# Performance work log

Hardware: AMD Instinct MI355X
Metric: run time of the kernel (lower is better)

Reference implementation:

```python
import jax, jax.numpy as jnp
import numpy as np

K = 5       # local window size (odd)
G = 4       # groups

def _gconv1x1(x, w):
    # grouped 1x1 conv: x (b,c,h,w), w (g, c_out_g, c_in_g) -> (b,g,c_out_g,h,w)
    b, c, h, wd = x.shape
    g, co, ci = w.shape
    xg = x.reshape(b, g, ci, h, wd)
    return jnp.einsum('bgihw,goi->bgohw', xg, w)

def _windows(f, h, w):
    # f: (b,g,n,h+2p,w+2p) -> (b,g,n,h,w,K*K), row-major over (ki,kj)
    # matches torch .unfold(2,K,1).unfold(3,K,1).view(..., -1)
    return jnp.stack([f[..., i:i + h, j:j + w]
                      for i in range(K) for j in range(K)], axis=-1)

def setup_inputs() -> dict:
    key = jax.random.key(0)
    k1, k2, k3, k4 = jax.random.split(key, 4)
    x = jax.random.normal(k1, (2, 128, 96, 96), dtype=jnp.float32)
    wq = jax.random.normal(k2, (G, 32, 32), dtype=jnp.float32) * 0.1
    wk = jax.random.normal(k3, (G, 32, 32), dtype=jnp.float32) * 0.1
    wv = jax.random.normal(k4, (G, 32, 32), dtype=jnp.float32) * 0.1
    return {"x": x, "wq": wq, "wk": wk, "wv": wv}

def reference(x, wq, wk, wv):
    b, c, h, w = x.shape
    p = K // 2
    # query: plain grouped 1x1 conv, broadcast over window dim
    q = _gconv1x1(x, wq)[..., None]                      # (b,g,n,h,w,1)
    # key/value: reflect-pad (1x1 conv commutes with padding, same as torch's
    # Conv2d(..., padding=k//2, padding_mode='reflect'))
    xp = jnp.pad(x, ((0, 0), (0, 0), (p, p), (p, p)), mode='reflect')
    kf = _gconv1x1(xp, wk)                               # (b,g,n,h+2p,w+2p)
    vf = _gconv1x1(xp, wv)
    kwin = _windows(kf, h, w)                            # (b,g,n,h,w,K*K)
    vwin = _windows(vf, h, w)
    attn = jax.nn.softmax(q * kwin, axis=-1)             # per-channel window softmax
    y = (attn * vwin).sum(-1)                            # (b,g,n,h,w)
    return y.reshape(b, -1, h, w)                        # (b, c_out, h, w)
```

## Files before the change

kernel.cpp:

```cpp
#include <hip/hip_runtime.h>


#define HW 96
#define RG 12
#define CSTR 36
#define PXN 9216

typedef _Float16 half8  __attribute__((ext_vector_type(8)));
typedef _Float16 half2v __attribute__((ext_vector_type(2)));
typedef float    float4v __attribute__((ext_vector_type(4)));
typedef unsigned int uint4v __attribute__((ext_vector_type(4)));

__device__ __forceinline__ int refl(int i) {
    i = (i < 0) ? -i : i;
    i = (i > 95) ? (190 - i) : i;
    return i;
}

__global__ __launch_bounds__(256) void conv_qkv(
    const float* __restrict__ x, const float* __restrict__ wq,
    const float* __restrict__ wk, const float* __restrict__ wv,
    _Float16* __restrict__ qp, _Float16* __restrict__ kp, _Float16* __restrict__ vp)
{
    const int tid  = threadIdx.x;
    const int g = blockIdx.y, b = blockIdx.z;
    const int lane = tid & 63, wid = tid >> 6;
    const int col  = lane & 15;
    const int quad = lane >> 4;
    const int koff = quad * 8;
    const int pxw  = blockIdx.x * 128 + wid * 32;
    const float* xg = x + (size_t)(b * 128 + g * 32) * PXN;
    const size_t plane = (size_t)(b * 4 + g) * PXN * 32;

    const float* wsrc[3] = {wq, wk, wv};
    half8 frag[6];
    #pragma unroll
    for (int T = 0; T < 6; T++) {
        const float* wr = wsrc[T >> 1] + (g * 32 + (T & 1) * 16 + col) * 32 + koff;
        float sc = (T < 2) ? 1.44269504f : 1.0f;
        #pragma unroll
        for (int j = 0; j < 8; j++) frag[T][j] = (_Float16)(wr[j] * sc);
    }

    _Float16* outp[3] = {qp, kp, vp};
    #pragma unroll
    for (int s = 0; s < 2; s++) {
        int apx = pxw + s * 16 + col;
        half8 a;
        #pragma unroll
        for (int j = 0; j < 8; j++)
            a[j] = (_Float16)xg[(koff + j) * PXN + apx];
        #pragma unroll
        for (int T = 0; T < 6; T++) {
            float4v d = {0.f, 0.f, 0.f, 0.f};
            d = __builtin_amdgcn_mfma_f32_16x16x32_f16(a, frag[T], d, 0, 0, 0);
            _Float16* pl = outp[T >> 1];
            #pragma unroll
            for (int r = 0; r < 4; r++) {
                int dpx = pxw + s * 16 + quad * 4 + r;
                pl[plane + (size_t)dpx * 32 + (T & 1) * 16 + col] = (_Float16)d[r];
            }
        }
    }
}

__global__ __launch_bounds__(256) void attn(
    const _Float16* __restrict__ qp, const _Float16* __restrict__ kp,
    const _Float16* __restrict__ vp, float* __restrict__ out)
{
    __shared__ unsigned int kvb[144 * CSTR];

    const int tid = threadIdx.x;
    const int g = blockIdx.y, b = blockIdx.z;
    const int h0 = (blockIdx.x / 12) * 8;
    const int w0 = (blockIdx.x % 12) * 8;
    const int lane = tid & 63, wid = tid >> 6, n0 = wid * 8;
    const int ty = lane >> 3, tx = lane & 7;
    const size_t plane = (size_t)(b * 4 + g) * PXN * 32;

    const int qpx = (h0 + ty) * HW + (w0 + tx);
    uint4v qu = *(const uint4v*)(qp + plane + (size_t)qpx * 32 + n0);

    const int wA  = min(max(w0 - 4, 0), 80);
    const int off = w0 - 2 - wA;
    #pragma unroll
    for (int it = 0; it < 3; it++) {
        int idx  = it * 256 + tid;
        int chunk = idx & 3, px_i = (idx >> 2) & 15, row = idx >> 6;
        int iy = refl(h0 + row - 2);
        size_t gaddr = plane + (size_t)(iy * HW + wA + px_i) * 32 + chunk * 8;
        uint4v kq = *(const uint4v*)(kp + gaddr);
        uint4v vq = *(const uint4v*)(vp + gaddr);
        int s = px_i - off;
        if (s >= 0 && s < RG) {
            int base = (row * RG + s) * CSTR + chunk * 8;
            #pragma unroll
            for (int e = 0; e < 4; e++) {
                kvb[base + 2 * e]     = __builtin_amdgcn_perm(vq[e], kq[e], 0x05040100);
                kvb[base + 2 * e + 1] = __builtin_amdgcn_perm(vq[e], kq[e], 0x07060302);
            }
        }
    }
    __syncthreads();

    if (off != 2) {
        const int left = (w0 == 0);
        #pragma unroll
        for (int it = 0; it < 3; it++) {
            int idx = it * 256 + tid;
            int ch = idx & 31, rr = idx >> 5;
            int row = rr >> 1, wc = rr & 1;
            int dst = left ? wc : (10 + wc);
            int src = left ? (4 - wc) : (8 - wc);
            kvb[(row * RG + dst) * CSTR + ch] = kvb[(row * RG + src) * CSTR + ch];
        }
        __syncthreads();
    }

    half8 qh = __builtin_bit_cast(half8, qu);
    float qf[8];
    #pragma unroll
    for (int c = 0; c < 8; c++) qf[c] = (float)qh[c];

    float den[8], num[8];
    #pragma unroll
    for (int c = 0; c < 8; c++) { den[c] = 0.f; num[c] = 0.f; }

    #pragma unroll
    for (int dy = 0; dy < 5; dy++) {
        const unsigned int* base = &kvb[((ty + dy) * RG + tx) * CSTR + n0];
        uint4v t0[5], t1[5];
        #pragma unroll
        for (int dx = 0; dx < 5; dx++) {
            t0[dx] = *(const uint4v*)(base + dx * CSTR);
            t1[dx] = *(const uint4v*)(base + dx * CSTR + 4);
        }
        #pragma unroll
        for (int dx = 0; dx < 5; dx++) {
            #pragma unroll
            for (int c = 0; c < 8; c++) {
                unsigned int u = (c < 4) ? t0[dx][c] : t1[dx][c - 4];
                half2v kv = __builtin_bit_cast(half2v, u);
                float e = __builtin_amdgcn_exp2f(qf[c] * (float)kv[0]);
                den[c] += e;
                num[c] = fmaf(e, (float)kv[1], num[c]);
            }
        }
    }

    float* outp = out + (size_t)((b * 128 + g * 32 + n0) * HW + (h0 + ty)) * HW + (w0 + tx);
    #pragma unroll
    for (int c = 0; c < 8; c++)
        outp[c * (HW * HW)] = num[c] * __builtin_amdgcn_rcpf(den[c]);
}

extern "C" void kernel_launch(void* const* d_in, const int* in_sizes, int n_in,
                              void* d_out, int out_size, void* d_ws, size_t ws_size,
                              hipStream_t stream) {
    const float* x  = (const float*)d_in[0];
    const float* wq = (const float*)d_in[1];
    const float* wk = (const float*)d_in[2];
    const float* wv = (const float*)d_in[3];
    float* out = (float*)d_out;

    const size_t PLSZ = (size_t)2 * 4 * PXN * 32;
    _Float16* qp = (_Float16*)d_ws;
    _Float16* kp = qp + PLSZ;
    _Float16* vp = kp + PLSZ;

    conv_qkv<<<dim3(72, 4, 2), 256, 0, stream>>>(x, wq, wk, wv, qp, kp, vp);
    attn<<<dim3(144, 4, 2), 256, 0, stream>>>(qp, kp, vp, out);
}
```

Measured before the change: 90.61 us.

## Fuse grouped 1x1 QKV projection into attention kernel via shared memory

Merges the projection and attention kernels into one. Each block computes the Q/K/V projection for its 12x16 haloed tile directly from x with MFMA and writes the results straight into shared memory, so the fp16 workspace round-trip and the second launch go away. In exchange, halo pixels are projected redundantly by neighbouring blocks, shared memory use grows with a float Q buffer, and the block loads x with strided reads. Q is now kept in fp32 rather than rounded to fp16.

```diff
diff --git a/kernel.cpp b/kernel.cpp
--- a/kernel.cpp
+++ b/kernel.cpp
@@ -4,6 +4,7 @@
 #define HW 96
 #define RG 12
 #define CSTR 36
+#define QSTR 33
 #define PXN 9216
 
 typedef _Float16 half8  __attribute__((ext_vector_type(8)));
@@ -17,87 +18,76 @@
     return i;
 }
 
-__global__ __launch_bounds__(256) void conv_qkv(
+__global__ __launch_bounds__(256) void fused_attn(
     const float* __restrict__ x, const float* __restrict__ wq,
     const float* __restrict__ wk, const float* __restrict__ wv,
-    _Float16* __restrict__ qp, _Float16* __restrict__ kp, _Float16* __restrict__ vp)
+    float* __restrict__ out)
 {
-    const int tid  = threadIdx.x;
+    __shared__ unsigned int kvb[144 * CSTR];
+    __shared__ float qbuf[144 * QSTR];
+
+    const int tid = threadIdx.x;
     const int g = blockIdx.y, b = blockIdx.z;
+    const int h0 = (blockIdx.x / 12) * 8;
+    const int w0 = (blockIdx.x % 12) * 8;
     const int lane = tid & 63, wid = tid >> 6;
-    const int col  = lane & 15;
-    const int quad = lane >> 4;
-    const int koff = quad * 8;
-    const int pxw  = blockIdx.x * 128 + wid * 32;
+    const int col = lane & 15, quad = lane >> 4, koff = quad * 8;
+    const int ty = lane >> 3, tx = lane & 7, n0 = wid * 8;
+
+    const int wA  = min(max(w0 - 4, 0), 80);
+    const int off = w0 - 2 - wA;
+
     const float* xg = x + (size_t)(b * 128 + g * 32) * PXN;
-    const size_t plane = (size_t)(b * 4 + g) * PXN * 32;
 
     const float* wsrc[3] = {wq, wk, wv};
     half8 frag[6];
     #pragma unroll
     for (int T = 0; T < 6; T++) {
         const float* wr = wsrc[T >> 1] + (g * 32 + (T & 1) * 16 + col) * 32 + koff;
+        float4v lo = *(const float4v*)(wr);
+        float4v hi = *(const float4v*)(wr + 4);
         float sc = (T < 2) ? 1.44269504f : 1.0f;
         #pragma unroll
-        for (int j = 0; j < 8; j++) frag[T][j] = (_Float16)(wr[j] * sc);
+        for (int j = 0; j < 4; j++) {
+            frag[T][j]     = (_Float16)(lo[j] * sc);
+            frag[T][j + 4] = (_Float16)(hi[j] * sc);
+        }
     }
 
-    _Float16* outp[3] = {qp, kp, vp};
+    float av[3][8];
     #pragma unroll
-    for (int s = 0; s < 2; s++) {
-        int apx = pxw + s * 16 + col;
+    for (int t = 0; t < 3; t++) {
+        int iy = refl(h0 + (wid * 3 + t) - 2);
+        const float* xr = xg + (size_t)iy * HW + wA + col;
+        #pragma unroll
+        for (int j = 0; j < 8; j++)
+            av[t][j] = xr[(size_t)(koff + j) * PXN];
+    }
+
+    #pragma unroll
+    for (int t = 0; t < 3; t++) {
+        const int row = wid * 3 + t;
         half8 a;
         #pragma unroll
-        for (int j = 0; j < 8; j++)
-            a[j] = (_Float16)xg[(koff + j) * PXN + apx];
+        for (int j = 0; j < 8; j++) a[j] = (_Float16)av[t][j];
         #pragma unroll
-        for (int T = 0; T < 6; T++) {
-            float4v d = {0.f, 0.f, 0.f, 0.f};
-            d = __builtin_amdgcn_mfma_f32_16x16x32_f16(a, frag[T], d, 0, 0, 0);
-            _Float16* pl = outp[T >> 1];
+        for (int hf = 0; hf < 2; hf++) {
+            float4v z = {0.f, 0.f, 0.f, 0.f};
+            float4v dq = __builtin_amdgcn_mfma_f32_16x16x32_f16(a, frag[hf],     z, 0, 0, 0);
+            float4v dk = __builtin_amdgcn_mfma_f32_16x16x32_f16(a, frag[2 + hf], z, 0, 0, 0);
+            float4v dv = __builtin_amdgcn_mfma_f32_16x16x32_f16(a, frag[4 + hf], z, 0, 0, 0);
+            const int ch = hf * 16 + col;
             #pragma unroll
             for (int r = 0; r < 4; r++) {
-                int dpx = pxw + s * 16 + quad * 4 + r;
-                pl[plane + (size_t)dpx * 32 + (T & 1) * 16 + col] = (_Float16)d[r];
-            }
-        }
-    }
-}
-
-__global__ __launch_bounds__(256) void attn(
-    const _Float16* __restrict__ qp, const _Float16* __restrict__ kp,
-    const _Float16* __restrict__ vp, float* __restrict__ out)
-{
-    __shared__ unsigned int kvb[144 * CSTR];
-
-    const int tid = threadIdx.x;
-    const int g = blockIdx.y, b = blockIdx.z;
-    const int h0 = (blockIdx.x / 12) * 8;
-    const int w0 = (blockIdx.x % 12) * 8;
-    const int lane = tid & 63, wid = tid >> 6, n0 = wid * 8;
-    const int ty = lane >> 3, tx = lane & 7;
-    const size_t plane = (size_t)(b * 4 + g) * PXN * 32;
-
-    const int qpx = (h0 + ty) * HW + (w0 + tx);
-    uint4v qu = *(const uint4v*)(qp + plane + (size_t)qpx * 32 + n0);
-
-    const int wA  = min(max(w0 - 4, 0), 80);
-    const int off = w0 - 2 - wA;
-    #pragma unroll
-    for (int it = 0; it < 3; it++) {
-        int idx  = it * 256 + tid;
-        int chunk = idx & 3, px_i = (idx >> 2) & 15, row = idx >> 6;
-        int iy = refl(h0 + row - 2);
-        size_t gaddr = plane + (size_t)(iy * HW + wA + px_i) * 32 + chunk * 8;
-        uint4v kq = *(const uint4v*)(kp + gaddr);
-        uint4v vq = *(const uint4v*)(vp + gaddr);
-        int s = px_i - off;
-        if (s >= 0 && s < RG) {
-            int base = (row * RG + s) * CSTR + chunk * 8;
-            #pragma unroll
-            for (int e = 0; e < 4; e++) {
-                kvb[base + 2 * e]     = __builtin_amdgcn_perm(vq[e], kq[e], 0x05040100);
-                kvb[base + 2 * e + 1] = __builtin_amdgcn_perm(vq[e], kq[e], 0x07060302);
+                int s = quad * 4 + r - off;
+                if (s >= 0 && s < RG) {
+                    int p = row * RG + s;
+                    half2v kv;
+                    kv[0] = (_Float16)dk[r];
+                    kv[1] = (_Float16)dv[r];
+                    kvb[p * CSTR + ch]  = __builtin_bit_cast(unsigned int, kv);
+                    qbuf[p * QSTR + ch] = dq[r];
+                }
             }
         }
     }
@@ -117,10 +107,12 @@
         __syncthreads();
     }
 
-    half8 qh = __builtin_bit_cast(half8, qu);
     float qf[8];
-    #pragma unroll
-    for (int c = 0; c < 8; c++) qf[c] = (float)qh[c];
+    {
+        const float* qb = &qbuf[((ty + 2) * RG + (tx + 2)) * QSTR + n0];
+        #pragma unroll
+        for (int c = 0; c < 8; c++) qf[c] = qb[c];
+    }
 
     float den[8], num[8];
     #pragma unroll
@@ -162,12 +154,7 @@
     const float* wk = (const float*)d_in[2];
     const float* wv = (const float*)d_in[3];
     float* out = (float*)d_out;
+    (void)d_ws; (void)ws_size;
 
-    const size_t PLSZ = (size_t)2 * 4 * PXN * 32;
-    _Float16* qp = (_Float16*)d_ws;
-    _Float16* kp = qp + PLSZ;
-    _Float16* vp = kp + PLSZ;
-
-    conv_qkv<<<dim3(72, 4, 2), 256, 0, stream>>>(x, wq, wk, wv, qp, kp, vp);
-    attn<<<dim3(144, 4, 2), 256, 0, stream>>>(qp, kp, vp, out);
+    fused_attn<<<dim3(144, 4, 2), 256, 0, stream>>>(x, wq, wk, wv, out);
 }
```

After: 91.33 us. Within noise of the previous version (+0.8%).
